# Performance work log

Measured on AMD Instinct MI355X. Metric: run time of the kernel, lower is better.

The kernel has to match this reference:

```python
import jax, jax.numpy as jnp
import numpy as np

EPS = 1e-5

def mvn(x):
    # per-(N,C) spatial mean/std normalization; torch .var is unbiased (ddof=1)
    mean = jnp.mean(x, axis=(2, 3), keepdims=True)
    var = jnp.var(x, axis=(2, 3), ddof=1, keepdims=True)
    return (x - mean) / jnp.sqrt(var + EPS)

def conv1x1(x, w, b):
    # w: [O, C] (1x1 conv collapsed), x: [B, C, H, W]
    return jnp.einsum('bchw,oc->bohw', x, w) + b[None, :, None, None]

def conv3x3(x, w, b):
    # w: [O, I, 3, 3], VALID padding (snet uses padding=0)
    y = jax.lax.conv_general_dilated(x, w, (1, 1), 'VALID',
                                     dimension_numbers=('NCHW', 'OIHW', 'NCHW'))
    return y + b[None, :, None, None]

def safe_cbrt(x):
    # pow(relu(x), 1/3) with safe gradient at 0 (forward identical)
    pos = x > 0
    return jnp.where(pos, jnp.power(jnp.where(pos, x, 1.0), 1.0 / 3.0), 0.0)

def _forward(content, style, wf_san, bf_san, wg_san, bg_san, wh_san, bh_san,
             wf_mcc, bf_mcc, wg_mcc, bg_mcc, w_fc, b_fc, w_out, b_out,
             wc1, bc1, wc2, bc2, wc3, bc3, ws1, bs1, ws2, bs2, ws3, bs3,
             w_unc, b_unc):
    B, C, H, W = content.shape
    cn = mvn(content)
    sn = mvn(style)

    # --- MCC branch: channel correlation statistic of style ---
    F_Fc = conv1x1(cn, wf_mcc, bf_mcc)                      # [B,C,H,W]
    g = conv1x1(sn, wg_mcc, bg_mcc).reshape(B, C, H * W)    # [B,C,HW]
    FC_S = jnp.sum(g * g, axis=-1) / jnp.sum(g, axis=-1)    # [B,C]
    FC_S = FC_S @ w_fc.T + b_fc                             # Linear
    part1 = F_Fc * FC_S[:, :, None, None]

    # --- WCT-like covariance branch (compressed 32-dim space) ---
    Fs0 = style - jnp.mean(style, axis=(2, 3), keepdims=True)  # nor_mean
    fc_ = conv1x1(jax.nn.relu(conv1x1(jax.nn.relu(conv1x1(cn, wc1, bc1)), wc2, bc2)), wc3, bc3)  # [B,32,H,W]
    fs_ = conv1x1(jax.nn.relu(conv3x3(jax.nn.relu(conv3x3(Fs0, ws1, bs1)), ws2, bs2)), ws3, bs3)  # [B,32,H-4,W-4]
    cdim = fc_.shape[1]
    fs_flat = fs_.reshape(B, cdim, -1)                       # [B,32,hw_s]
    cov = jnp.einsum('bci,bdi->bcd', fs_flat, fs_flat) / fs_flat.shape[2]  # [B,32,32]
    out = jnp.einsum('bcd,bdi->bci', cov, fc_.reshape(B, cdim, H * W)).reshape(B, cdim, H, W)
    part2 = conv1x1(out, w_unc, b_unc)                       # [B,512,H,W]

    # --- SANet-style attention branch ---
    F_s = conv1x1(cn, wf_san, bf_san).reshape(B, C, H * W)
    G_s = conv1x1(sn, wg_san, bg_san).reshape(B, C, H * W)
    H_s = conv1x1(style, wh_san, bh_san).reshape(B, C, H * W)
    S = jax.nn.softmax(jnp.einsum('bci,bcj->bij', F_s, G_s), axis=-1)  # [B,HW,HW]
    part3 = jnp.einsum('bcj,bij->bci', H_s, S).reshape(B, C, H, W)

    p = safe_cbrt(jax.nn.relu(part1 * part2 * part3))
    return conv1x1(p, w_out, b_out) + content


def setup_inputs() -> dict:
    key = jax.random.key(0)
    B, C, H, W = 16, 512, 32, 32
    s = 0.02
    shapes = {
        'content': (B, C, H, W), 'style': (B, C, H, W),
        'wf_san': (C, C), 'bf_san': (C,), 'wg_san': (C, C), 'bg_san': (C,),
        'wh_san': (C, C), 'bh_san': (C,),
        'wf_mcc': (C, C), 'bf_mcc': (C,), 'wg_mcc': (C, C), 'bg_mcc': (C,),
        'w_fc': (C, C), 'b_fc': (C,), 'w_out': (C, C), 'b_out': (C,),
        'wc1': (256, 512), 'bc1': (256,), 'wc2': (128, 256), 'bc2': (128,),
        'wc3': (32, 128), 'bc3': (32,),
        'ws1': (256, 512, 3, 3), 'bs1': (256,), 'ws2': (128, 256, 3, 3), 'bs2': (128,),
        'ws3': (32, 128), 'bs3': (32,),
        'w_unc': (512, 32), 'b_unc': (512,),
    }
    d = {}
    for i, (name, shp) in enumerate(shapes.items()):
        k = jax.random.fold_in(key, i)
        scale = 1.0 if name in ('content', 'style') else s
        d[name] = jax.random.normal(k, shp, dtype=jnp.float32) * scale
    return d


def reference(content, style, wf_san, bf_san, wg_san, bg_san, wh_san, bh_san,
              wf_mcc, bf_mcc, wg_mcc, bg_mcc, w_fc, b_fc, w_out, b_out,
              wc1, bc1, wc2, bc2, wc3, bc3, ws1, bs1, ws2, bs2, ws3, bs3,
              w_unc, b_unc):
    return _forward(content, style, wf_san, bf_san, wg_san, bg_san, wh_san, bh_san,
                    wf_mcc, bf_mcc, wg_mcc, bg_mcc, w_fc, b_fc, w_out, b_out,
                    wc1, bc1, wc2, bc2, wc3, bc3, ws1, bs1, ws2, bs2, ws3, bs3,
                    w_unc, b_unc)
```

## Files before the change

kernel.cpp:

```cpp
#include <hip/hip_runtime.h>
#include <hip/hip_bf16.h>
#include <hip/hip_fp16.h>
#include <math.h>


typedef __attribute__((ext_vector_type(8))) short short8;
typedef __attribute__((ext_vector_type(4))) float f32x4;
typedef unsigned short us;
#define MFMA16 __builtin_amdgcn_mfma_f32_16x16x32_bf16

struct h16 { us v; };

template <class A, class B> struct SameT { static constexpr bool v = false; };
template <class A> struct SameT<A, A> { static constexpr bool v = true; };

__device__ inline float b2f(us b) { return __uint_as_float(((unsigned)b) << 16); }
__device__ inline us f2b(float f) {
    unsigned u = __float_as_uint(f);
    return (us)((u + 0x7FFFu + ((u >> 16) & 1u)) >> 16);
}

template <typename TOUT>
__device__ inline us cvt2b(float x) {
    if constexpr (SameT<TOUT, h16>::v) return __half_as_ushort(__float2half(x));
    else return f2b(x);
}

__device__ inline double blockReduceSumD(double v, double* sh) {
    int t = threadIdx.x;
    sh[t] = v; __syncthreads();
    for (int s = blockDim.x >> 1; s > 0; s >>= 1) {
        if (t < s) sh[t] += sh[t + s];
        __syncthreads();
    }
    double r = sh[0]; __syncthreads();
    return r;
}

__global__ __launch_bounds__(256) void stats_k(const float* __restrict__ X,
                                               float* __restrict__ mean,
                                               float* __restrict__ inv, int HW) {
    __shared__ double sh[256];
    int bc = blockIdx.x;
    const float* x = X + (size_t)bc * HW;
    int t = threadIdx.x;
    float v[4];
    double s = 0.0;
    #pragma unroll
    for (int r = 0; r < 4; ++r) { v[r] = x[t + r * 256]; s += (double)v[r]; }
    double tot = blockReduceSumD(s, sh);
    double ss = 0.0;
    #pragma unroll
    for (int r = 0; r < 4; ++r) ss += (double)v[r] * (double)v[r];
    double tot2 = blockReduceSumD(ss, sh);
    if (t == 0) {
        double m = tot / HW;
        double var = (tot2 - tot * tot / HW) / (HW - 1);
        mean[bc] = (float)m;
        inv[bc] = (float)(1.0 / sqrt(var + 1e-5));
    }
}

__global__ __launch_bounds__(256) void trn_k(const float* __restrict__ X,
                                             const float* __restrict__ mean,
                                             const float* __restrict__ inv,
                                             us* __restrict__ Yn, us* __restrict__ Yc,
                                             us* __restrict__ Yr, int C, int HW) {
    __shared__ us Ln[64 * 65];
    __shared__ us Lc[64 * 65];
    __shared__ us Lr[64 * 65];
    int bz = blockIdx.z, c0 = blockIdx.y * 64, h0 = blockIdx.x * 64;
    const float* Xb = X + (size_t)bz * C * HW;
    int t = threadIdx.x;
    int cl = t >> 3, h8 = (t & 7) * 8;
    #pragma unroll
    for (int half = 0; half < 2; ++half) {
        int c = cl + half * 32;
        int gc = c0 + c;
        float m = mean[bz * C + gc], iv = inv[bz * C + gc];
        const float4* s4 = (const float4*)&Xb[(size_t)gc * HW + h0 + h8];
        float4 f0 = s4[0], f1 = s4[1];
        float vv[8] = {f0.x, f0.y, f0.z, f0.w, f1.x, f1.y, f1.z, f1.w};
        #pragma unroll
        for (int i = 0; i < 8; ++i) {
            int li = c * 65 + h8 + i;
            if (Yn) Ln[li] = f2b((vv[i] - m) * iv);
            if (Yc) Lc[li] = f2b(vv[i] - m);
            if (Yr) Lr[li] = f2b(vv[i]);
        }
    }
    __syncthreads();
    int hl = t >> 3, c8 = (t & 7) * 8;
    #pragma unroll
    for (int half = 0; half < 2; ++half) {
        int hh = hl + half * 32;
        size_t off = ((size_t)bz * HW + h0 + hh) * (size_t)C + c0 + c8;
        us tmp[8];
        if (Yn) {
            #pragma unroll
            for (int i = 0; i < 8; ++i) tmp[i] = Ln[(c8 + i) * 65 + hh];
            *(uint4*)&Yn[off] = *(const uint4*)tmp;
        }
        if (Yc) {
            #pragma unroll
            for (int i = 0; i < 8; ++i) tmp[i] = Lc[(c8 + i) * 65 + hh];
            *(uint4*)&Yc[off] = *(const uint4*)tmp;
        }
        if (Yr) {
            #pragma unroll
            for (int i = 0; i < 8; ++i) tmp[i] = Lr[(c8 + i) * 65 + hh];
            *(uint4*)&Yr[off] = *(const uint4*)tmp;
        }
    }
}

template <typename TE>
__device__ inline void stage16(const TE* __restrict__ src, bool valid, us* dst) {
    us tmp[16];
    if (valid) {
        if constexpr (sizeof(TE) == 2) {
            uint4 a = ((const uint4*)src)[0], b = ((const uint4*)src)[1];
            *(uint4*)&tmp[0] = a; *(uint4*)&tmp[8] = b;
        } else {
            const float4* s4 = (const float4*)src;
            float4 f0 = s4[0], f1 = s4[1], f2 = s4[2], f3 = s4[3];
            float vv[16] = {f0.x, f0.y, f0.z, f0.w, f1.x, f1.y, f1.z, f1.w,
                            f2.x, f2.y, f2.z, f2.w, f3.x, f3.y, f3.z, f3.w};
            #pragma unroll
            for (int i = 0; i < 16; ++i) tmp[i] = f2b(vv[i]);
        }
    } else {
        #pragma unroll
        for (int i = 0; i < 16; ++i) tmp[i] = 0;
    }
    ((uint4*)dst)[0] = *(uint4*)&tmp[0];
    ((uint4*)dst)[1] = *(uint4*)&tmp[8];
}

template <typename TAel, typename TBel, typename TOUT, int OUTT>
__global__ __launch_bounds__(256) void mf2_k(const TAel* __restrict__ A, long astride, int lda,
                                             const TBel* __restrict__ B, long bstride, int ldb,
                                             const float* __restrict__ bias,
                                             TOUT* __restrict__ Y,
                                             const float* __restrict__ add_src,
                                             int K, int M, int N, int relu) {
    __shared__ __align__(16) us smem[20480];
    int bz = blockIdx.z;
    int mbase = blockIdx.y * 128, nbase = blockIdx.x * 128;
    const TAel* Ab = A + (size_t)bz * astride;
    const TBel* Bb = B + (size_t)bz * bstride;
    int t = threadIdx.x;
    int row = t & 127, kh = t >> 7;
    int wave = t >> 6, lane = t & 63, lm = lane & 15, q = lane >> 4;
    int mh = (wave >> 1) * 64, nh = (wave & 1) * 64;
    int gm = mbase + row, gn = nbase + row;
    bool vm = gm < M, vn = gn < N;

    auto As = [&](int buf) { return smem + buf * 5120; };
    auto Bs = [&](int buf) { return smem + 10240 + buf * 5120; };

    auto stage = [&](int buf, int kb) {
        stage16(Ab + (size_t)gm * lda + kb + kh * 16, vm, As(buf) + row * 40 + kh * 16);
        stage16(Bb + (size_t)gn * ldb + kb + kh * 16, vn, Bs(buf) + row * 40 + kh * 16);
    };

    f32x4 acc[4][4];
    #pragma unroll
    for (int i = 0; i < 4; ++i)
        #pragma unroll
        for (int j = 0; j < 4; ++j) acc[i][j] = (f32x4){0.f, 0.f, 0.f, 0.f};

    stage(0, 0);
    __syncthreads();
    int cur = 0;
    for (int kb = 0; kb < K; kb += 32) {
        if (kb + 32 < K) stage(cur ^ 1, kb + 32);
        short8 af[4], bf[4];
        #pragma unroll
        for (int i = 0; i < 4; ++i) af[i] = *(const short8*)(As(cur) + (mh + i * 16 + lm) * 40 + q * 8);
        #pragma unroll
        for (int j = 0; j < 4; ++j) bf[j] = *(const short8*)(Bs(cur) + (nh + j * 16 + lm) * 40 + q * 8);
        #pragma unroll
        for (int i = 0; i < 4; ++i)
            #pragma unroll
            for (int j = 0; j < 4; ++j)
                acc[i][j] = MFMA16(af[i], bf[j], acc[i][j], 0, 0, 0);
        __syncthreads();
        cur ^= 1;
    }

    if constexpr (sizeof(TOUT) == 2) {
        if (mbase + 128 <= M && nbase + 128 <= N) {
            us* Ts = smem;
            #pragma unroll
            for (int i = 0; i < 4; ++i) {
                int m0 = mh + i * 16 + q * 4;
                float bv[4];
                #pragma unroll
                for (int r = 0; r < 4; ++r) bv[r] = bias ? bias[mbase + m0 + r] : 0.f;
                #pragma unroll
                for (int j = 0; j < 4; ++j) {
                    int nl = nh + j * 16 + lm;
                    #pragma unroll
                    for (int r = 0; r < 4; ++r) {
                        float x = acc[i][j][r] + bv[r];
                        if (relu) x = (x > 0.f) ? x : 0.f;
                        us val = cvt2b<TOUT>(x);
                        if (OUTT == 0) Ts[(m0 + r) * 136 + nl] = val;
                        else Ts[nl * 136 + m0 + r] = val;
                    }
                }
            }
            __syncthreads();
            #pragma unroll
            for (int k2 = 0; k2 < 8; ++k2) {
                int flat = k2 * 256 + t;
                int r0 = flat >> 4, u = flat & 15;
                uint4 vv = *(const uint4*)&Ts[r0 * 136 + u * 8];
                us* dst;
                if (OUTT == 0)
                    dst = (us*)&Y[((size_t)bz * M + mbase + r0) * N + nbase + u * 8];
                else
                    dst = (us*)&Y[((size_t)bz * N + nbase + r0) * M + mbase + u * 8];
                *(uint4*)dst = vv;
            }
            return;
        }
    }

    #pragma unroll
    for (int i = 0; i < 4; ++i) {
        int m0 = mbase + mh + i * 16 + q * 4;
        if (m0 >= M) continue;
        float bv[4];
        #pragma unroll
        for (int r = 0; r < 4; ++r) bv[r] = bias ? bias[m0 + r] : 0.f;
        #pragma unroll
        for (int j = 0; j < 4; ++j) {
            int n = nbase + nh + j * 16 + lm;
            if (n >= N) continue;
            float v[4];
            #pragma unroll
            for (int r = 0; r < 4; ++r) {
                float x = acc[i][j][r] + bv[r];
                if (relu) x = (x > 0.f) ? x : 0.f;
                v[r] = x;
            }
            if (OUTT == 1) {
                size_t off = ((size_t)bz * N + n) * (size_t)M + m0;
                if constexpr (sizeof(TOUT) == 2) {
                    us o4[4];
                    #pragma unroll
                    for (int r = 0; r < 4; ++r) o4[r] = cvt2b<TOUT>(v[r]);
                    *(uint2*)&Y[off] = *(const uint2*)o4;
                } else {
                    float4 f4 = make_float4(v[0], v[1], v[2], v[3]);
                    *(float4*)&Y[off] = f4;
                }
            } else {
                #pragma unroll
                for (int r = 0; r < 4; ++r) {
                    size_t off = ((size_t)bz * M + m0 + r) * (size_t)N + n;
                    float x = v[r];
                    if (add_src) x += add_src[off];
                    if constexpr (sizeof(TOUT) == 2) {
                        us val = cvt2b<TOUT>(x);
                        *(us*)&Y[off] = val;
                    } else Y[off] = x;
                }
            }
        }
    }
}

struct SBias {
    const float* bp[10];
    int moff[10];
    unsigned relu;
};
__global__ __launch_bounds__(256) void mfs_k(const us* __restrict__ A,
                                             const us* __restrict__ B, long bstride, int ldb,
                                             us* __restrict__ Y, int ldy,
                                             SBias sb, int K, int N) {
    __shared__ __align__(16) us smem[20480];
    int bz = blockIdx.z;
    int mbase = blockIdx.y * 128, nbase = blockIdx.x * 128;
    const us* Bb = B + (size_t)bz * bstride;
    int t = threadIdx.x;
    int row = t & 127, kh = t >> 7;
    int wave = t >> 6, lane = t & 63, lm = lane & 15, q = lane >> 4;
    int mh = (wave >> 1) * 64, nh = (wave & 1) * 64;
    int relu = (sb.relu >> blockIdx.y) & 1;
    const float* bias = sb.bp[blockIdx.y];
    int moff = sb.moff[blockIdx.y];

    auto As = [&](int buf) { return smem + buf * 5120; };
    auto Bs = [&](int buf) { return smem + 10240 + buf * 5120; };

    auto stage = [&](int buf, int kb) {
        stage16(A + (size_t)(mbase + row) * K + kb + kh * 16, true, As(buf) + row * 40 + kh * 16);
        stage16(Bb + (size_t)(nbase + row) * ldb + kb + kh * 16, true, Bs(buf) + row * 40 + kh * 16);
    };

    f32x4 acc[4][4];
    #pragma unroll
    for (int i = 0; i < 4; ++i)
        #pragma unroll
        for (int j = 0; j < 4; ++j) acc[i][j] = (f32x4){0.f, 0.f, 0.f, 0.f};

    stage(0, 0);
    __syncthreads();
    int cur = 0;
    for (int kb = 0; kb < K; kb += 32) {
        if (kb + 32 < K) stage(cur ^ 1, kb + 32);
        short8 af[4], bf[4];
        #pragma unroll
        for (int i = 0; i < 4; ++i) af[i] = *(const short8*)(As(cur) + (mh + i * 16 + lm) * 40 + q * 8);
        #pragma unroll
        for (int j = 0; j < 4; ++j) bf[j] = *(const short8*)(Bs(cur) + (nh + j * 16 + lm) * 40 + q * 8);
        #pragma unroll
        for (int i = 0; i < 4; ++i)
            #pragma unroll
            for (int j = 0; j < 4; ++j)
                acc[i][j] = MFMA16(af[i], bf[j], acc[i][j], 0, 0, 0);
        __syncthreads();
        cur ^= 1;
    }

    us* Ts = smem;
    #pragma unroll
    for (int i = 0; i < 4; ++i) {
        int m0 = mh + i * 16 + q * 4;
        float bv[4];
        #pragma unroll
        for (int r = 0; r < 4; ++r) bv[r] = bias[mbase + m0 - moff + r];
        #pragma unroll
        for (int j = 0; j < 4; ++j) {
            int nl = nh + j * 16 + lm;
            #pragma unroll
            for (int r = 0; r < 4; ++r) {
                float x = acc[i][j][r] + bv[r];
                if (relu) x = (x > 0.f) ? x : 0.f;
                Ts[nl * 136 + m0 + r] = f2b(x);
            }
        }
    }
    __syncthreads();
    #pragma unroll
    for (int k2 = 0; k2 < 8; ++k2) {
        int flat = k2 * 256 + t;
        int r0 = flat >> 4, u = flat & 15;
        uint4 vv = *(const uint4*)&Ts[r0 * 136 + u * 8];
        *(uint4*)&Y[((size_t)bz * N + nbase + r0) * ldy + mbase + u * 8] = vv;
    }
}

struct CpyArg {
    const float* src[11];
    unsigned long long dstoff[11];
    int len[11];
};
__global__ __launch_bounds__(256) void wcat_k(CpyArg a, us* __restrict__ arena) {
    int seg = blockIdx.y;
    int idx = blockIdx.x * 256 + threadIdx.x;
    if (idx < a.len[seg]) arena[a.dstoff[seg] + idx] = f2b(a.src[seg][idx]);
}

__global__ __launch_bounds__(256) void reorder_wf_k(const float* __restrict__ W,
                                                    us* __restrict__ Wf, int O, int Cin) {
    int idx = blockIdx.x * 256 + threadIdx.x;
    int OT = O >> 6, KB = Cin >> 5;
    int total = OT * KB * 9 * 4 * 64;
    if (idx >= total) return;
    int lane = idx & 63;
    int f = idx >> 6;
    int i = f & 1, half = (f >> 1) & 1;
    int tf = f >> 2;
    int tap = tf % 9;
    int rest = tf / 9;
    int kb = rest % KB, ot = rest / KB;
    int o = ot * 64 + half * 32 + i * 16 + (lane & 15);
    int cb = kb * 32 + (lane >> 4) * 8;
    us v[8];
    #pragma unroll
    for (int e = 0; e < 8; ++e)
        v[e] = f2b(W[((size_t)o * Cin + cb + e) * 9 + tap]);
    *(uint4*)&Wf[(size_t)idx * 8] = *(const uint4*)v;
}

template <int PR>
__device__ inline void stage_patch(const us* __restrict__ Xb, us* __restrict__ dst,
                                   int pyb, int kb, int Cin, int IH, int IW, int t) {
    const int ITEMS = (2 * PR + 2) * 36 * 4;
    for (int i = t; i < ITEMS; i += 256) {
        int p = i >> 2, q8 = (i & 3) * 8;
        int r = p / 36, x = p - r * 36;
        int gy = pyb + r;
        uint4 v = make_uint4(0u, 0u, 0u, 0u);
        if (x < IW && gy < IH)
            v = *(const uint4*)&Xb[((size_t)(gy * IW + x)) * Cin + kb * 32 + q8];
        *(uint4*)&dst[p * 40 + q8] = v;
    }
}

template <int PR>
__global__ __launch_bounds__(256) void conv_mf4_k(const us* __restrict__ X, long xbstride,
                                                  const us* __restrict__ Wf,
                                                  const float* __restrict__ bias,
                                                  us* __restrict__ Y, long ybstride,
                                                  int Cin, int O, int IH, int IW,
                                                  int OH, int OW) {
    __shared__ us patch[2][(2 * PR + 2) * 36 * 40];
    int bz = blockIdx.z;
    int obase = blockIdx.y * 64;
    int pyb = blockIdx.x * (2 * PR);
    const us* Xb = X + (size_t)bz * xbstride;
    int t = threadIdx.x;
    int wave = t >> 6, lane = t & 63, lm = lane & 15, q = lane >> 4;
    int half = wave >> 1, rw = wave & 1;
    int KB = Cin >> 5;
    const us* Wb = Wf + (size_t)(obase >> 6) * KB * 9 * 2048;

    f32x4 acc[PR][2][2];
    #pragma unroll
    for (int pr = 0; pr < PR; ++pr)
        #pragma unroll
        for (int i = 0; i < 2; ++i)
            #pragma unroll
            for (int j = 0; j < 2; ++j) acc[pr][i][j] = (f32x4){0.f, 0.f, 0.f, 0.f};

    stage_patch<PR>(Xb, patch[0], pyb, 0, Cin, IH, IW, t);
    __syncthreads();
    int cur = 0;
    for (int kb = 0; kb < KB; ++kb) {
        if (kb + 1 < KB) stage_patch<PR>(Xb, patch[cur ^ 1], pyb, kb + 1, Cin, IH, IW, t);
        const us* Wk = Wb + (size_t)kb * 9 * 2048;
        #pragma unroll
        for (int tap = 0; tap < 9; ++tap) {
            int ky = tap / 3, kx = tap - ky * 3;
            const us* wt = Wk + tap * 2048 + half * 1024;
            short8 a0 = *(const short8*)&wt[lane * 8];
            short8 a1 = *(const short8*)&wt[512 + lane * 8];
            #pragma unroll
            for (int pr = 0; pr < PR; ++pr) {
                int prow = (pr * 2 + rw + ky) * 36;
                short8 b0 = *(const short8*)&patch[cur][(prow + lm + kx) * 40 + q * 8];
                short8 b1 = *(const short8*)&patch[cur][(prow + 16 + lm + kx) * 40 + q * 8];
                acc[pr][0][0] = MFMA16(a0, b0, acc[pr][0][0], 0, 0, 0);
                acc[pr][0][1] = MFMA16(a0, b1, acc[pr][0][1], 0, 0, 0);
                acc[pr][1][0] = MFMA16(a1, b0, acc[pr][1][0], 0, 0, 0);
                acc[pr][1][1] = MFMA16(a1, b1, acc[pr][1][1], 0, 0, 0);
            }
        }
        __syncthreads();
        cur ^= 1;
    }

    us* Yb = Y + (size_t)bz * ybstride;
    #pragma unroll
    for (int pr = 0; pr < PR; ++pr) {
        int py = pyb + pr * 2 + rw;
        if (py >= OH) continue;
        #pragma unroll
        for (int i = 0; i < 2; ++i) {
            int m0 = obase + half * 32 + i * 16 + q * 4;
            #pragma unroll
            for (int j = 0; j < 2; ++j) {
                int px = j * 16 + lm;
                if (px >= OW) continue;
                us o4[4];
                #pragma unroll
                for (int r = 0; r < 4; ++r) {
                    float v = acc[pr][i][j][r] + bias[m0 + r];
                    v = (v > 0.f) ? v : 0.f;
                    o4[r] = f2b(v);
                }
                *(uint2*)&Yb[((size_t)(py * OW + px)) * O + m0] = *(const uint2*)o4;
            }
        }
    }
}

__global__ __launch_bounds__(256) void gemm_k(const float* __restrict__ W,
                                              const float* __restrict__ X,
                                              const float* __restrict__ bias,
                                              float* __restrict__ Y,
                                              int C, int O, int N) {
    int obase = blockIdx.y * 32;
    __shared__ float As[32][33];
    __shared__ float Bs[32][33];
    int t = threadIdx.x;
    int tx = t & 15, ty = t >> 4;
    float acc00 = 0, acc01 = 0, acc10 = 0, acc11 = 0;
    for (int cb = 0; cb < C; cb += 32) {
        int k = t & 31, o0 = t >> 5;
        #pragma unroll
        for (int r = 0; r < 4; ++r) {
            int ol = o0 + r * 8;
            As[k][ol] = W[(size_t)(obase + ol) * C + cb + k];
        }
        int n0 = t & 31, k0 = t >> 5;
        #pragma unroll
        for (int r = 0; r < 4; ++r) {
            int k2 = k0 + r * 8;
            Bs[k2][n0] = (n0 < N) ? X[(size_t)(cb + k2) * N + n0] : 0.f;
        }
        __syncthreads();
        #pragma unroll
        for (int k2 = 0; k2 < 32; ++k2) {
            float a0 = As[k2][ty], a1 = As[k2][ty + 16];
            float b0 = Bs[k2][tx], b1 = Bs[k2][tx + 16];
            acc00 += a0 * b0; acc01 += a0 * b1;
            acc10 += a1 * b0; acc11 += a1 * b1;
        }
        __syncthreads();
    }
    float accs[2][2] = {{acc00, acc01}, {acc10, acc11}};
    #pragma unroll
    for (int i = 0; i < 2; ++i) {
        int o = obase + ty + i * 16;
        float bv = bias[o];
        #pragma unroll
        for (int j = 0; j < 2; ++j) {
            int n = tx + j * 16;
            if (n < N) Y[(size_t)o * N + n] = accs[i][j] + bv;
        }
    }
}

__global__ __launch_bounds__(256) void fcs3a_k(const us* __restrict__ g, int ldg,
                                               float* __restrict__ pa, int HW) {
    int b = blockIdx.x, j = blockIdx.y;
    int t = threadIdx.x;
    const us* gb = g + ((size_t)b * HW + (size_t)j * 128) * ldg + 2 * t;
    double s0 = 0.0, s1 = 0.0;
    #pragma unroll 4
    for (int hw = 0; hw < 128; ++hw) {
        unsigned u = *(const unsigned*)&gb[(size_t)hw * ldg];
        float f0 = b2f((us)(u & 0xFFFFu));
        float f1 = b2f((us)(u >> 16));
        s0 += (double)f0 * (double)f0;
        s1 += (double)f1 * (double)f1;
    }
    float2 w = make_float2((float)s0, (float)s1);
    *(float2*)&pa[((size_t)b * 8 + j) * 512 + 2 * t] = w;
}

__global__ __launch_bounds__(256) void fcs3b_k(const float* __restrict__ pa,
                                               const float* __restrict__ bg,
                                               float* __restrict__ fcs, int B, int HW) {
    int b = blockIdx.x;
    int t = threadIdx.x;
    double s0 = 0.0, s1 = 0.0;
    #pragma unroll
    for (int j = 0; j < 8; ++j) {
        float2 w = *(const float2*)&pa[((size_t)b * 8 + j) * 512 + 2 * t];
        s0 += (double)w.x; s1 += (double)w.y;
    }
    int c0 = 2 * t;
    fcs[(size_t)c0 * B + b] = (float)(s0 / ((double)HW * (double)bg[c0]));
    fcs[(size_t)(c0 + 1) * B + b] = (float)(s1 / ((double)HW * (double)bg[c0 + 1]));
}

__global__ __launch_bounds__(256) void softmax_k(const us* __restrict__ S,
                                                 us* __restrict__ P) {
    __shared__ float sh[256];
    size_t row = blockIdx.x;
    const us* r = S + row * 1024;
    us* po = P + row * 1024;
    int t = threadIdx.x;
    us raw[4];
    *(uint2*)raw = *(const uint2*)&r[t * 4];
    float v[4];
    float m = -INFINITY;
    #pragma unroll
    for (int i = 0; i < 4; ++i) {
        v[i] = __half2float(__ushort_as_half(raw[i]));
        m = fmaxf(m, v[i]);
    }
    sh[t] = m; __syncthreads();
    for (int s = 128; s > 0; s >>= 1) { if (t < s) sh[t] = fmaxf(sh[t], sh[t + s]); __syncthreads(); }
    m = sh[0]; __syncthreads();
    float sum = 0;
    #pragma unroll
    for (int i = 0; i < 4; ++i) { v[i] = expf(v[i] - m); sum += v[i]; }
    sh[t] = sum; __syncthreads();
    for (int s = 128; s > 0; s >>= 1) { if (t < s) sh[t] += sh[t + s]; __syncthreads(); }
    float inv = 1.f / sh[0]; __syncthreads();
    #pragma unroll
    for (int i = 0; i < 4; ++i) raw[i] = f2b(v[i] * inv);
    *(uint2*)&po[t * 4] = *(const uint2*)raw;
}

__global__ __launch_bounds__(256) void cov2_k(const float* __restrict__ fs,
                                              float* __restrict__ cov, int Cd, int M) {
    __shared__ float Ls[196 * 36];
    int bb = blockIdx.x;
    int t = threadIdx.x;
    const float* p = fs + (size_t)bb * M * Cd;
    int c = t >> 3, d0 = (t & 7) * 4;
    float a0 = 0.f, a1 = 0.f, a2 = 0.f, a3 = 0.f;
    for (int ch = 0; ch < 4; ++ch) {
        __syncthreads();
        for (int i = t; i < 1568; i += 256) {
            int rowi = i >> 3, c4 = (i & 7) * 4;
            float4 v = *(const float4*)&p[(size_t)(ch * 196 + rowi) * Cd + c4];
            *(float4*)&Ls[rowi * 36 + c4] = v;
        }
        __syncthreads();
        for (int i = 0; i < 196; ++i) {
            float a = Ls[i * 36 + c];
            a0 += a * Ls[i * 36 + d0 + 0];
            a1 += a * Ls[i * 36 + d0 + 1];
            a2 += a * Ls[i * 36 + d0 + 2];
            a3 += a * Ls[i * 36 + d0 + 3];
        }
    }
    float invM = 1.f / (float)M;
    size_t base = ((size_t)bb * Cd + c) * Cd + d0;
    cov[base + 0] = a0 * invM;
    cov[base + 1] = a1 * invM;
    cov[base + 2] = a2 * invM;
    cov[base + 3] = a3 * invM;
}

__global__ __launch_bounds__(256) void fuse_k(const us* __restrict__ ffc, int ldf,
                                              const float* __restrict__ fc2t,
                                              const us* __restrict__ p2,
                                              const us* __restrict__ p3,
                                              us* __restrict__ out, int B, int C, int HW) {
    size_t idx = (size_t)blockIdx.x * 256 + threadIdx.x;
    size_t total = (size_t)B * C * HW;
    if (idx >= total) return;
    int c = (int)(idx & (size_t)(C - 1));
    size_t tok = idx >> 9;
    int b = (int)(idx / ((size_t)C * HW));
    float part1 = b2f(ffc[tok * ldf + c]) * fc2t[(size_t)c * B + b];
    float v = part1 * b2f(p2[idx]) * b2f(p3[idx]);
    v = (v > 0.f) ? v : 0.f;
    out[idx] = f2b(cbrtf(v));
}

extern "C" void kernel_launch(void* const* d_in, const int* in_sizes, int n_in,
                              void* d_out, int out_size, void* d_ws, size_t ws_size,
                              hipStream_t stream) {
    typedef const float* fp;
    fp content = (fp)d_in[0];
    fp style   = (fp)d_in[1];
    fp wf_san = (fp)d_in[2],  bf_san = (fp)d_in[3];
    fp wg_san = (fp)d_in[4],  bg_san = (fp)d_in[5];
    fp wh_san = (fp)d_in[6],  bh_san = (fp)d_in[7];
    fp wf_mcc = (fp)d_in[8],  bf_mcc = (fp)d_in[9];
    fp wg_mcc = (fp)d_in[10], bg_mcc = (fp)d_in[11];
    fp w_fc   = (fp)d_in[12], b_fc   = (fp)d_in[13];
    fp w_out  = (fp)d_in[14], b_out  = (fp)d_in[15];
    fp wc1 = (fp)d_in[16], bc1 = (fp)d_in[17];
    fp wc2 = (fp)d_in[18], bc2 = (fp)d_in[19];
    fp wc3 = (fp)d_in[20], bc3 = (fp)d_in[21];
    fp ws1 = (fp)d_in[22], bs1 = (fp)d_in[23];
    fp ws2 = (fp)d_in[24], bs2 = (fp)d_in[25];
    fp ws3 = (fp)d_in[26], bs3 = (fp)d_in[27];
    fp w_unc = (fp)d_in[28], b_unc = (fp)d_in[29];

    const int B = 16, C = 512, HW = 1024;
    const size_t NE = (size_t)B * C * HW;
    const long TOK = (long)C * HW;
    const size_t MB = 1u << 20;
    char* base = (char*)d_ws;

    us* cnT      = (us*)(base);
    us* snT      = (us*)(base + 16 * MB);
    us* fs0T     = (us*)(base + 32 * MB);
    us* s1       = (us*)(base + 48 * MB);
    us* s2       = (us*)(base + 56 * MB);
    float* fs_c  = (float*)(base + 60 * MB);
    us* Sbuf16   = (us*)(base);
    h16* Sh      = (h16*)(base);
    us* cnOut    = (us*)(base + 64 * MB);
    us* snOut    = (us*)(base + 104 * MB);
    us* part3b   = (us*)(base + 104 * MB);
    us* part2b   = (us*)(base + 120 * MB);
    us* Pb       = (us*)(base + 136 * MB);
    us* t2b      = (us*)(base + 136 * MB);
    float* fc_c  = (float*)(base + 140 * MB);
    float* out32 = (float*)(base + 142 * MB);
    us* pbuf     = (us*)(base + 144 * MB);
    us* styleT   = (us*)(base + 168 * MB);
    us* Hco      = (us*)(base + 184 * MB);

    char* misc = base + 200 * MB;
    us* Wr1   = (us*)(misc);
    us* Wr2   = (us*)(misc + 2359296);
    us* arena = (us*)(misc + 2949120);
    us* Wcn   = arena;
    us* Wsn   = arena + 655360;
    us* Wh    = arena + 1179648;
    us* Wout  = arena + 1441792;
    us* Wc2   = arena + 1703936;
    us* Wc3   = arena + 1736704;
    us* Ws3   = arena + 1740800;
    us* Wunc  = arena + 1744896;
    float* pa    = (float*)(misc + 6471680);
    float* fcs   = (float*)(misc + 6733824);
    float* fc2t  = (float*)(misc + 6766592);
    float* cov   = (float*)(misc + 6799360);
    float* meanC = (float*)(misc + 6864896);
    float* invC  = (float*)(misc + 6897664);
    float* meanS = (float*)(misc + 6930432);
    float* invS  = (float*)(misc + 6963200);

    CpyArg ca;
    const float* srcs[11] = {wf_mcc, wc1, wf_san, wg_mcc, wg_san, wh_san,
                             w_out, wc2, wc3, ws3, w_unc};
    int lens[11] = {262144, 131072, 262144, 262144, 262144, 262144,
                    262144, 32768, 4096, 4096, 16384};
    unsigned long long off = 0;
    for (int i = 0; i < 11; ++i) { ca.src[i] = srcs[i]; ca.dstoff[i] = off; ca.len[i] = lens[i]; off += lens[i]; }
    wcat_k<<<dim3(1024, 11), 256, 0, stream>>>(ca, arena);
    reorder_wf_k<<<576, 256, 0, stream>>>(ws1, Wr1, 256, 512);
    reorder_wf_k<<<72, 256, 0, stream>>>(ws2, Wr2, 128, 256);

    stats_k<<<B * C, 256, 0, stream>>>(content, meanC, invC, HW);
    stats_k<<<B * C, 256, 0, stream>>>(style, meanS, invS, HW);
    trn_k<<<dim3(16, 8, 16), 256, 0, stream>>>(content, meanC, invC, cnT, nullptr, nullptr, C, HW);
    trn_k<<<dim3(16, 8, 16), 256, 0, stream>>>(style, meanS, invS, snT, fs0T, styleT, C, HW);

    conv_mf4_k<1><<<dim3(15, 4, 16), 256, 0, stream>>>(fs0T, TOK, Wr1, bs1,
                                                       s1, (long)900 * 256, 512, 256, 32, 32, 30, 30);
    conv_mf4_k<1><<<dim3(14, 2, 16), 256, 0, stream>>>(s1, (long)900 * 256, Wr2, bs2,
                                                       s2, (long)784 * 128, 256, 128, 30, 30, 28, 28);
    mf2_k<us, us, float, 1><<<dim3(7, 1, 16), 256, 0, stream>>>(
        Ws3, 0, 128, s2, (long)784 * 128, 128, bs3, fs_c, nullptr, 128, 32, 784, 0);
    cov2_k<<<B, 256, 0, stream>>>(fs_c, cov, 32, 784);

    {
        SBias sb;
        for (int y = 0; y < 4; ++y) { sb.bp[y] = bf_mcc; sb.moff[y] = 0; }
        for (int y = 4; y < 6; ++y) { sb.bp[y] = bc1; sb.moff[y] = 512; }
        for (int y = 6; y < 10; ++y) { sb.bp[y] = bf_san; sb.moff[y] = 768; }
        sb.relu = 0x030u;
        mfs_k<<<dim3(8, 10, 16), 256, 0, stream>>>(Wcn, cnT, TOK, 512, cnOut, 1280, sb, 512, 1024);
    }

    {
        SBias sb;
        for (int y = 0; y < 4; ++y) { sb.bp[y] = bg_mcc; sb.moff[y] = 0; }
        for (int y = 4; y < 8; ++y) { sb.bp[y] = bg_san; sb.moff[y] = 512; }
        for (int y = 8; y < 10; ++y) { sb.bp[y] = bg_mcc; sb.moff[y] = 0; }
        sb.relu = 0u;
        mfs_k<<<dim3(8, 8, 16), 256, 0, stream>>>(Wsn, snT, TOK, 512, snOut, 1024, sb, 512, 1024);
    }

    fcs3a_k<<<dim3(B, 8), 256, 0, stream>>>(snOut, 1024, pa, HW);
    fcs3b_k<<<B, 256, 0, stream>>>(pa, bg_mcc, fcs, B, HW);
    gemm_k<<<dim3(1, 16, 1), 256, 0, stream>>>(w_fc, fcs, b_fc, fc2t, 512, 512, 16);

    mf2_k<us, us, us, 0><<<dim3(8, 4, 16), 256, 0, stream>>>(
        Wh, 0, 512, styleT, TOK, 512, bh_san, Hco, nullptr, 512, 512, 1024, 0);

    mf2_k<us, us, h16, 0><<<dim3(8, 8, 16), 256, 0, stream>>>(
        cnOut + 768, (long)1024 * 1280, 1280, snOut + 512, (long)1024 * 1024, 1024,
        nullptr, Sh, nullptr, 512, 1024, 1024, 0);
    softmax_k<<<B * HW, 256, 0, stream>>>(Sbuf16, Pb);

    mf2_k<us, us, us, 0><<<dim3(4, 8, 16), 256, 0, stream>>>(
        Pb, (long)1024 * 1024, 1024, Hco, TOK, 1024, nullptr, part3b, nullptr,
        1024, 1024, 512, 0);

    mf2_k<us, us, us, 1><<<dim3(8, 1, 16), 256, 0, stream>>>(
        Wc2, 0, 256, cnOut + 512, (long)1024 * 1280, 1280, bc2, t2b, nullptr, 256, 128, 1024, 1);
    mf2_k<us, us, float, 1><<<dim3(8, 1, 16), 256, 0, stream>>>(
        Wc3, 0, 128, t2b, (long)1024 * 128, 128, bc3, fc_c, nullptr, 128, 32, 1024, 0);

    mf2_k<float, float, float, 1><<<dim3(8, 1, 16), 256, 0, stream>>>(
        cov, 1024, 32, fc_c, (long)1024 * 32, 32, nullptr, out32, nullptr, 32, 32, 1024, 0);
    mf2_k<us, float, us, 1><<<dim3(8, 4, 16), 256, 0, stream>>>(
        Wunc, 0, 32, out32, (long)1024 * 32, 32, b_unc, part2b, nullptr, 32, 512, 1024, 0);

    fuse_k<<<(unsigned)((NE + 255) / 256), 256, 0, stream>>>(
        cnOut, 1280, fc2t, part2b, part3b, pbuf, B, C, HW);

    mf2_k<us, us, float, 0><<<dim3(8, 4, 16), 256, 0, stream>>>(
        Wout, 0, 512, pbuf, TOK, 512, b_out, (float*)d_out, content, 512, 512, 1024, 0);
}
```

Before: 751.2 us.

## Pre-swizzle GEMM weights into MFMA fragment order and load them directly

Adds a kernel that rearranges each bf16 weight matrix into per-lane MFMA fragment order. It also adds a new GEMM kernel that reads these weight fragments straight from global memory, so only the activation operand is staged through LDS. This halves shared memory per block and removes the LDS write/read round trip for the weight tile. In exchange the weight loads are no longer prefetched, and several extra reorder launches run on every call. The new kernel replaces the fused content/style projections, the H projection, Wc2, Wunc and the output projection.

```diff
diff --git a/kernel.cpp b/kernel.cpp
--- a/kernel.cpp
+++ b/kernel.cpp
@@ -278,28 +278,47 @@
     int moff[10];
     unsigned relu;
 };
-__global__ __launch_bounds__(256) void mfs_k(const us* __restrict__ A,
-                                             const us* __restrict__ B, long bstride, int ldb,
-                                             us* __restrict__ Y, int ldy,
-                                             SBias sb, int K, int N) {
-    __shared__ __align__(16) us smem[20480];
-    int bz = blockIdx.z;
-    int mbase = blockIdx.y * 128, nbase = blockIdx.x * 128;
-    const us* Bb = B + (size_t)bz * bstride;
+
+__global__ __launch_bounds__(256) void reorder_gw_k(const us* __restrict__ W,
+                                                    us* __restrict__ Wf, int M, int K) {
+    int idx = blockIdx.x * 256 + threadIdx.x;
+    int KB = K >> 5;
+    int total = (M >> 7) * KB * 8 * 64;
+    if (idx >= total) return;
+    int lane = idx & 63;
+    int f = idx >> 6;
+    int i = f & 3, mhalf = (f >> 2) & 1;
+    int rest = f >> 3;
+    int kb = rest % KB, mt = rest / KB;
+    int row = mt * 128 + mhalf * 64 + i * 16 + (lane & 15);
+    int col = kb * 32 + (lane >> 4) * 8;
+    *(uint4*)&Wf[(size_t)idx * 8] = *(const uint4*)&W[(size_t)row * K + col];
+}
+
+template <typename TBel, typename TOUT, int OUTT>
+__global__ __launch_bounds__(256) void mfw_k(const us* __restrict__ Wf,
+                                             const TBel* __restrict__ B, long bstride, int ldb,
+                                             TOUT* __restrict__ Y, int ldy,
+                                             SBias sb, const float* __restrict__ add_src,
+                                             int K, int M, int N) {
+    __shared__ __align__(16) us smem[10240];
+    int bz = blockIdx.z, mt = blockIdx.y;
+    int mbase = mt * 128, nbase = blockIdx.x * 128;
+    const TBel* Bb = B + (size_t)bz * bstride;
     int t = threadIdx.x;
     int row = t & 127, kh = t >> 7;
     int wave = t >> 6, lane = t & 63, lm = lane & 15, q = lane >> 4;
-    int mh = (wave >> 1) * 64, nh = (wave & 1) * 64;
-    int relu = (sb.relu >> blockIdx.y) & 1;
-    const float* bias = sb.bp[blockIdx.y];
-    int moff = sb.moff[blockIdx.y];
-
-    auto As = [&](int buf) { return smem + buf * 5120; };
-    auto Bs = [&](int buf) { return smem + 10240 + buf * 5120; };
-
-    auto stage = [&](int buf, int kb) {
-        stage16(A + (size_t)(mbase + row) * K + kb + kh * 16, true, As(buf) + row * 40 + kh * 16);
-        stage16(Bb + (size_t)(nbase + row) * ldb + kb + kh * 16, true, Bs(buf) + row * 40 + kh * 16);
+    int mhalf = wave >> 1, nh = (wave & 1) * 64;
+    int KB = K >> 5;
+    const us* Wb = Wf + (size_t)mt * KB * 4096;
+    int relu = (sb.relu >> mt) & 1;
+    const float* bias = sb.bp[mt];
+    int moff = sb.moff[mt];
+
+    auto Bs = [&](int buf) { return smem + buf * 5120; };
+    auto stageB = [&](int buf, int kb) {
+        stage16(Bb + (size_t)(nbase + row) * ldb + (size_t)kb * 32 + kh * 16, true,
+                Bs(buf) + row * 40 + kh * 16);
     };
 
     f32x4 acc[4][4];
@@ -308,14 +327,15 @@
         #pragma unroll
         for (int j = 0; j < 4; ++j) acc[i][j] = (f32x4){0.f, 0.f, 0.f, 0.f};
 
-    stage(0, 0);
+    stageB(0, 0);
     __syncthreads();
     int cur = 0;
-    for (int kb = 0; kb < K; kb += 32) {
-        if (kb + 32 < K) stage(cur ^ 1, kb + 32);
+    for (int kb = 0; kb < KB; ++kb) {
+        if (kb + 1 < KB) stageB(cur ^ 1, kb + 1);
+        const us* wk = Wb + (size_t)kb * 4096 + mhalf * 2048;
         short8 af[4], bf[4];
         #pragma unroll
-        for (int i = 0; i < 4; ++i) af[i] = *(const short8*)(As(cur) + (mh + i * 16 + lm) * 40 + q * 8);
+        for (int i = 0; i < 4; ++i) af[i] = *(const short8*)&wk[i * 512 + lane * 8];
         #pragma unroll
         for (int j = 0; j < 4; ++j) bf[j] = *(const short8*)(Bs(cur) + (nh + j * 16 + lm) * 40 + q * 8);
         #pragma unroll
@@ -327,31 +347,67 @@
         cur ^= 1;
     }
 
-    us* Ts = smem;
-    #pragma unroll
-    for (int i = 0; i < 4; ++i) {
-        int m0 = mh + i * 16 + q * 4;
-        float bv[4];
-        #pragma unroll
-        for (int r = 0; r < 4; ++r) bv[r] = bias[mbase + m0 - moff + r];
-        #pragma unroll
-        for (int j = 0; j < 4; ++j) {
-            int nl = nh + j * 16 + lm;
-            #pragma unroll
-            for (int r = 0; r < 4; ++r) {
-                float x = acc[i][j][r] + bv[r];
-                if (relu) x = (x > 0.f) ? x : 0.f;
-                Ts[nl * 136 + m0 + r] = f2b(x);
+    if constexpr (sizeof(TOUT) == 2) {
+        us* Ts = smem;
+        #pragma unroll
+        for (int p = 0; p < 2; ++p) {
+            bool part = (OUTT == 1) ? ((wave & 1) == p) : (mhalf == p);
+            if (part) {
+                #pragma unroll
+                for (int i = 0; i < 4; ++i) {
+                    int m0 = mhalf * 64 + i * 16 + q * 4;
+                    float bv[4];
+                    #pragma unroll
+                    for (int r = 0; r < 4; ++r) bv[r] = bias[mbase + m0 + r - moff];
+                    #pragma unroll
+                    for (int j = 0; j < 4; ++j) {
+                        int nl = nh + j * 16 + lm;
+                        #pragma unroll
+                        for (int r = 0; r < 4; ++r) {
+                            float x = acc[i][j][r] + bv[r];
+                            if (relu) x = (x > 0.f) ? x : 0.f;
+                            us val = cvt2b<TOUT>(x);
+                            if (OUTT == 1) Ts[(nl - p * 64) * 136 + m0 + r] = val;
+                            else Ts[(m0 + r - p * 64) * 136 + nl] = val;
+                        }
+                    }
+                }
             }
-        }
-    }
-    __syncthreads();
-    #pragma unroll
-    for (int k2 = 0; k2 < 8; ++k2) {
-        int flat = k2 * 256 + t;
-        int r0 = flat >> 4, u = flat & 15;
-        uint4 vv = *(const uint4*)&Ts[r0 * 136 + u * 8];
-        *(uint4*)&Y[((size_t)bz * N + nbase + r0) * ldy + mbase + u * 8] = vv;
+            __syncthreads();
+            #pragma unroll
+            for (int k2 = 0; k2 < 4; ++k2) {
+                int flat = k2 * 256 + t;
+                int r0 = flat >> 4, u = flat & 15;
+                uint4 vv = *(const uint4*)&Ts[r0 * 136 + u * 8];
+                us* dst;
+                if (OUTT == 1)
+                    dst = (us*)&Y[((size_t)bz * N + nbase + p * 64 + r0) * ldy + mbase + u * 8];
+                else
+                    dst = (us*)&Y[((size_t)bz * M + mbase + p * 64 + r0) * (size_t)N + nbase + u * 8];
+                *(uint4*)dst = vv;
+            }
+            __syncthreads();
+        }
+    } else {
+        #pragma unroll
+        for (int i = 0; i < 4; ++i) {
+            int m0 = mbase + mhalf * 64 + i * 16 + q * 4;
+            float bv[4];
+            #pragma unroll
+            for (int r = 0; r < 4; ++r) bv[r] = bias[m0 + r - moff];
+            #pragma unroll
+            for (int j = 0; j < 4; ++j) {
+                int n = nbase + nh + j * 16 + lm;
+                #pragma unroll
+                for (int r = 0; r < 4; ++r) {
+                    size_t off = ((size_t)bz * M + m0 + r) * (size_t)N + n;
+                    float x = acc[i][j][r] + bv[r];
+                    if (relu) x = (x > 0.f) ? x : 0.f;
+                    if (add_src) x += add_src[off];
+                    Y[off] = x;
+                }
+            }
+        }
     }
 }
 
@@ -708,6 +764,12 @@
     float* invC  = (float*)(misc + 6897664);
     float* meanS = (float*)(misc + 6930432);
     float* invS  = (float*)(misc + 6963200);
+    us* Fcn  = (us*)(misc + 6995968);
+    us* Fsn  = (us*)(misc + 8306688);
+    us* Fh   = (us*)(misc + 9355264);
+    us* Fout = (us*)(misc + 9879552);
+    us* Fc2  = (us*)(misc + 10403840);
+    us* Func = (us*)(misc + 10469376);
 
     CpyArg ca;
     const float* srcs[11] = {wf_mcc, wc1, wf_san, wg_mcc, wg_san, wh_san,
@@ -719,6 +781,12 @@
     wcat_k<<<dim3(1024, 11), 256, 0, stream>>>(ca, arena);
     reorder_wf_k<<<576, 256, 0, stream>>>(ws1, Wr1, 256, 512);
     reorder_wf_k<<<72, 256, 0, stream>>>(ws2, Wr2, 128, 256);
+    reorder_gw_k<<<320, 256, 0, stream>>>(Wcn, Fcn, 1280, 512);
+    reorder_gw_k<<<256, 256, 0, stream>>>(Wsn, Fsn, 1024, 512);
+    reorder_gw_k<<<128, 256, 0, stream>>>(Wh, Fh, 512, 512);
+    reorder_gw_k<<<128, 256, 0, stream>>>(Wout, Fout, 512, 512);
+    reorder_gw_k<<<16, 256, 0, stream>>>(Wc2, Fc2, 128, 256);
+    reorder_gw_k<<<8, 256, 0, stream>>>(Wunc, Func, 512, 32);
 
     stats_k<<<B * C, 256, 0, stream>>>(content, meanC, invC, HW);
     stats_k<<<B * C, 256, 0, stream>>>(style, meanS, invS, HW);
@@ -739,7 +807,8 @@
         for (int y = 4; y < 6; ++y) { sb.bp[y] = bc1; sb.moff[y] = 512; }
         for (int y = 6; y < 10; ++y) { sb.bp[y] = bf_san; sb.moff[y] = 768; }
         sb.relu = 0x030u;
-        mfs_k<<<dim3(8, 10, 16), 256, 0, stream>>>(Wcn, cnT, TOK, 512, cnOut, 1280, sb, 512, 1024);
+        mfw_k<us, us, 1><<<dim3(8, 10, 16), 256, 0, stream>>>(
+            Fcn, cnT, TOK, 512, cnOut, 1280, sb, nullptr, 512, 1280, 1024);
     }
 
     {
@@ -748,15 +817,21 @@
         for (int y = 4; y < 8; ++y) { sb.bp[y] = bg_san; sb.moff[y] = 512; }
         for (int y = 8; y < 10; ++y) { sb.bp[y] = bg_mcc; sb.moff[y] = 0; }
         sb.relu = 0u;
-        mfs_k<<<dim3(8, 8, 16), 256, 0, stream>>>(Wsn, snT, TOK, 512, snOut, 1024, sb, 512, 1024);
+        mfw_k<us, us, 1><<<dim3(8, 8, 16), 256, 0, stream>>>(
+            Fsn, snT, TOK, 512, snOut, 1024, sb, nullptr, 512, 1024, 1024);
     }
 
     fcs3a_k<<<dim3(B, 8), 256, 0, stream>>>(snOut, 1024, pa, HW);
     fcs3b_k<<<B, 256, 0, stream>>>(pa, bg_mcc, fcs, B, HW);
     gemm_k<<<dim3(1, 16, 1), 256, 0, stream>>>(w_fc, fcs, b_fc, fc2t, 512, 512, 16);
 
-    mf2_k<us, us, us, 0><<<dim3(8, 4, 16), 256, 0, stream>>>(
-        Wh, 0, 512, styleT, TOK, 512, bh_san, Hco, nullptr, 512, 512, 1024, 0);
+    {
+        SBias sb;
+        for (int y = 0; y < 10; ++y) { sb.bp[y] = bh_san; sb.moff[y] = 0; }
+        sb.relu = 0u;
+        mfw_k<us, us, 0><<<dim3(8, 4, 16), 256, 0, stream>>>(
+            Fh, styleT, TOK, 512, Hco, 0, sb, nullptr, 512, 512, 1024);
+    }
 
     mf2_k<us, us, h16, 0><<<dim3(8, 8, 16), 256, 0, stream>>>(
         cnOut + 768, (long)1024 * 1280, 1280, snOut + 512, (long)1024 * 1024, 1024,
@@ -767,19 +842,34 @@
         Pb, (long)1024 * 1024, 1024, Hco, TOK, 1024, nullptr, part3b, nullptr,
         1024, 1024, 512, 0);
 
-    mf2_k<us, us, us, 1><<<dim3(8, 1, 16), 256, 0, stream>>>(
-        Wc2, 0, 256, cnOut + 512, (long)1024 * 1280, 1280, bc2, t2b, nullptr, 256, 128, 1024, 1);
+    {
+        SBias sb;
+        for (int y = 0; y < 10; ++y) { sb.bp[y] = bc2; sb.moff[y] = 0; }
+        sb.relu = 0x1u;
+        mfw_k<us, us, 1><<<dim3(8, 1, 16), 256, 0, stream>>>(
+            Fc2, cnOut + 512, (long)1024 * 1280, 1280, t2b, 128, sb, nullptr, 256, 128, 1024);
+    }
     mf2_k<us, us, float, 1><<<dim3(8, 1, 16), 256, 0, stream>>>(
         Wc3, 0, 128, t2b, (long)1024 * 128, 128, bc3, fc_c, nullptr, 128, 32, 1024, 0);
 
     mf2_k<float, float, float, 1><<<dim3(8, 1, 16), 256, 0, stream>>>(
         cov, 1024, 32, fc_c, (long)1024 * 32, 32, nullptr, out32, nullptr, 32, 32, 1024, 0);
-    mf2_k<us, float, us, 1><<<dim3(8, 4, 16), 256, 0, stream>>>(
-        Wunc, 0, 32, out32, (long)1024 * 32, 32, b_unc, part2b, nullptr, 32, 512, 1024, 0);
+    {
+        SBias sb;
+        for (int y = 0; y < 10; ++y) { sb.bp[y] = b_unc; sb.moff[y] = 0; }
+        sb.relu = 0u;
+        mfw_k<float, us, 1><<<dim3(8, 4, 16), 256, 0, stream>>>(
+            Func, out32, (long)1024 * 32, 32, part2b, 512, sb, nullptr, 32, 512, 1024);
+    }
 
     fuse_k<<<(unsigned)((NE + 255) / 256), 256, 0, stream>>>(
         cnOut, 1280, fc2t, part2b, part3b, pbuf, B, C, HW);
 
-    mf2_k<us, us, float, 0><<<dim3(8, 4, 16), 256, 0, stream>>>(
-        Wout, 0, 512, pbuf, TOK, 512, b_out, (float*)d_out, content, 512, 512, 1024, 0);
-}
+    {
+        SBias sb;
+        for (int y = 0; y < 10; ++y) { sb.bp[y] = b_out; sb.moff[y] = 0; }
+        sb.relu = 0u;
+        mfw_k<us, float, 0><<<dim3(8, 4, 16), 256, 0, stream>>>(
+            Fout, pbuf, TOK, 512, (float*)d_out, 0, sb, content, 512, 512, 1024);
+    }
+}
```

New measurement: 754.3 us. No clear change (+0.4%).
